# Kernel optimization log

Measured on AMD Instinct MI355X. Metric: run time of the kernel, lower is better.

The kernel has to match this reference:

```python
import jax, jax.numpy as jnp
import numpy as np

B, LQ, LK, H = 8, 2048, 2048, 1024


def setup_inputs() -> dict:
    key = jax.random.key(0)
    kq, kk, kv, km, kw = jax.random.split(key, 5)
    input_Q = jax.random.normal(kq, (B, LQ, H), dtype=jnp.float32)
    input_K = jax.random.normal(kk, (B, LK, H), dtype=jnp.float32)
    input_V = jax.random.normal(kv, (B, LK, H), dtype=jnp.float32)
    mask = jax.random.randint(km, (B, LK), 0, 2, dtype=jnp.int32)
    # learned parameter w_omega [H, H]; scaled init so scores are O(1)-ish
    w_omega = jax.random.normal(kw, (H, H), dtype=jnp.float32) * (H ** -0.5)
    return {"input_Q": input_Q, "input_K": input_K, "input_V": input_V,
            "w_omega": w_omega, "mask": mask}


def reference(input_Q, input_K, input_V, w_omega, mask):
    # att_input = Q @ W : [B, Lq, H]
    att_input = jnp.einsum('bqh,hd->bqd', input_Q, w_omega)
    # scores = att_input @ K^T : [B, Lq, Lk]
    att_scores = jnp.einsum('bqd,bkd->bqk', att_input, input_K)
    # masked fill with -inf where mask == 0 (mask broadcast over query dim)
    neg_inf = jnp.asarray(-jnp.inf, dtype=att_scores.dtype)
    scores = jnp.where(mask[:, None, :] == 0, neg_inf, att_scores)
    probs_softmax = jax.nn.softmax(scores, axis=-1)          # [B, Lq, Lk]
    probs_sigmoid = jax.nn.sigmoid(scores)                   # sigmoid(-inf)=0
    probs_sigmoid_hat = (probs_sigmoid > 0.5).astype(probs_softmax.dtype)
    att_output_softmax = jnp.einsum('bqk,bkh->bqh', probs_softmax, input_V)
    att_output_sigmoid = jnp.einsum('bqk,bkh->bqh', probs_sigmoid_hat, input_V)
    # torch .squeeze(1) is a no-op here since Lq > 1
    return (att_output_softmax, att_output_sigmoid, probs_softmax, probs_sigmoid)
```

## Files before the change

### kernel.cpp

```cpp
#include <hip/hip_runtime.h>
#include <math.h>

#define B_  8
#define LQ_ 2048
#define LK_ 2048
#define H_  1024

#define TAU      4e-3f
#define FIX_CAP  32768
#define FIX_E    8
#define SCL      256.0f
#define SCLQ     16.0f
#define INV_SS   (1.0f / 1048576.0f)

#define KBLK 512

typedef unsigned short ushort_t;
typedef __attribute__((ext_vector_type(8))) _Float16 v8h;
typedef __attribute__((ext_vector_type(8))) short  v8s;
typedef __attribute__((ext_vector_type(4))) float  v4f;
typedef __attribute__((ext_vector_type(4))) float  f4;
typedef __attribute__((ext_vector_type(4))) int    i4;
typedef __attribute__((ext_vector_type(4))) short  s4;

#if defined(__has_builtin)
#if __has_builtin(__builtin_amdgcn_global_load_lds)
#define HAS_GLDS 1
#endif
#endif

__device__ __forceinline__ ushort_t f2bf(float x) {
  unsigned u = __float_as_uint(x);
  u = (u + 0x7FFFu + ((u >> 16) & 1u)) >> 16;
  return (ushort_t)u;
}
__device__ __forceinline__ void split2h(float x, ushort_t& h, ushort_t& l) {
  union { _Float16 f; ushort_t u; } a, b;
  a.f = (_Float16)x;
  b.f = (_Float16)(x - (float)a.f);
  h = a.u; l = b.u;
}

__device__ __forceinline__ void gld_lds16(void* lds_dst, const void* g_src) {
#ifdef HAS_GLDS
  __builtin_amdgcn_global_load_lds((const __attribute__((address_space(1))) void*)g_src,
                                   (__attribute__((address_space(3))) void*)lds_dst,
                                   16, 0, 0);
#else
  *(i4*)lds_dst = *(const i4*)g_src;
#endif
}

__device__ __forceinline__ void xcd_remap(int& bx, int& by, int& bz) {
  const int nx = gridDim.x, ny = gridDim.y;
  const int nwg = nx * ny * gridDim.z;
  const int hwid = bx + nx * (by + ny * bz);
  const int work = (hwid & 7) * (nwg >> 3) + (hwid >> 3);
  bx = work % nx;
  const int t = work / nx;
  by = t % ny;
  bz = t / ny;
}

#define WAIT_VM(n) asm volatile("s_waitcnt vmcnt(" #n ")" ::: "memory")

__global__ __launch_bounds__(256)
void k_prep(const float* __restrict__ Q, const float* __restrict__ K,
            const float* __restrict__ W, const float* __restrict__ V,
            ushort_t* __restrict__ Qhi, ushort_t* __restrict__ Qlo,
            ushort_t* __restrict__ Khi, ushort_t* __restrict__ Klo,
            ushort_t* __restrict__ Wthi, ushort_t* __restrict__ Wtlo,
            ushort_t* __restrict__ Vt, int* __restrict__ cnt) {
  const int blk = blockIdx.x;
  const int tid = threadIdx.x;
  if (blk == 0 && tid == 0) *cnt = 0;

  if (blk < 4096) {
    const int sb = blk & 2047;
    const float* x = (blk < 2048) ? Q : K;
    ushort_t* hi = (blk < 2048) ? Qhi : Khi;
    ushort_t* lo = (blk < 2048) ? Qlo : Klo;
    const float scale = (blk < 2048) ? SCLQ : SCL;
    const int n4 = (int)((size_t)B_ * LQ_ * H_ / 4);
    for (int i = sb * 256 + tid; i < n4; i += 2048 * 256) {
      f4 v = ((const f4*)x)[i];
      s4 h, l;
#pragma unroll
      for (int j = 0; j < 4; j++) {
        ushort_t hb, lb; split2h(v[j] * scale, hb, lb);
        h[j] = (short)hb; l[j] = (short)lb;
      }
      ((s4*)hi)[i] = h;
      ((s4*)lo)[i] = l;
    }
    return;
  }

  __shared__ float t[32][33];
  const int tx = tid & 31, ty = tid >> 5;
  int bx, by, bz, R, C, SPLIT;
  const float* X;
  float scale;
  if (blk < 5120) {
    const int wb = blk - 4096;
    bx = wb & 31; by = wb >> 5; bz = 0; R = H_; C = H_; SPLIT = 1; X = W; scale = SCL;
  } else {
    const int vb = blk - 5120;
    bx = vb & 31; by = (vb >> 5) & 63; bz = vb >> 11; R = LK_; C = H_; SPLIT = 0; X = V; scale = 1.0f;
  }
  const float* Xb = X + (size_t)bz * R * C;
  const int c0 = bx * 32, r0 = by * 32;
#pragma unroll
  for (int i = 0; i < 4; i++)
    t[ty + 8 * i][tx] = Xb[(size_t)(r0 + ty + 8 * i) * C + c0 + tx];
  __syncthreads();
#pragma unroll
  for (int i = 0; i < 4; i++) {
    float v = t[tx][ty + 8 * i] * scale;
    size_t o = (size_t)(c0 + ty + 8 * i) * R + r0 + tx;
    if (SPLIT) {
      ushort_t h, l; split2h(v, h, l);
      Wthi[o] = h; Wtlo[o] = l;
    } else {
      (Vt + (size_t)bz * R * C)[o] = f2bf(v);
    }
  }
}


template <int EPI>
__global__ __launch_bounds__(512, 1)
void gemm_hx2p(const ushort_t* __restrict__ Ahi, const ushort_t* __restrict__ Alo,
               const ushort_t* __restrict__ Bhi, const ushort_t* __restrict__ Blo,
               int KD, long strideAB, long strideBB, int N,
               ushort_t* __restrict__ OutHi, ushort_t* __restrict__ OutLo, long strideOB,
               float* __restrict__ S, float* __restrict__ G, ushort_t* __restrict__ Hatb,
               const int* __restrict__ mask, int* __restrict__ cnt, int* __restrict__ flist) {
  int bx = blockIdx.x, by = blockIdx.y, bz = blockIdx.z;
  xcd_remap(bx, by, bz);
  const int b  = bz;
  const int m0 = by * 256;
  const int n0 = bx * 256;
  const ushort_t* Ah = Ahi + (size_t)b * strideAB + (size_t)m0 * KD;
  const ushort_t* Al = Alo + (size_t)b * strideAB + (size_t)m0 * KD;
  const ushort_t* Bh = Bhi + (size_t)b * strideBB + (size_t)n0 * KD;
  const ushort_t* Bl = Blo + (size_t)b * strideBB + (size_t)n0 * KD;

  __shared__ __attribute__((aligned(16))) char lds[2 * 65536];

  const int tid  = threadIdx.x;
  const int lane = tid & 63;
  const int w    = tid >> 6;
  const int wm   = (w >> 2) * 128;
  const int wn   = (w & 3) * 64;
  const int fr   = lane & 15;
  const int cq   = lane >> 4;

  v4f acc[8][4] = {};

  const int r4 = tid >> 2;
  const int gc = (tid & 3) ^ ((r4 >> 1) & 3);
  const size_t go1 = (size_t)r4 * KD + gc * 8;
  const size_t go2 = (size_t)(r4 + 128) * KD + gc * 8;
  const int lo16 = tid * 16;

#define STG_HX(t_) do {                                                  \
    char* sb_ = lds + ((t_) & 1) * 65536;                                \
    const int kk_ = (t_) * 32;                                           \
    gld_lds16(sb_ + lo16,          Ah + go1 + kk_);                      \
    gld_lds16(sb_ + 8192  + lo16,  Ah + go2 + kk_);                      \
    gld_lds16(sb_ + 16384 + lo16,  Al + go1 + kk_);                      \
    gld_lds16(sb_ + 24576 + lo16,  Al + go2 + kk_);                      \
    gld_lds16(sb_ + 32768 + lo16,  Bh + go1 + kk_);                      \
    gld_lds16(sb_ + 40960 + lo16,  Bh + go2 + kk_);                      \
    gld_lds16(sb_ + 49152 + lo16,  Bl + go1 + kk_);                      \
    gld_lds16(sb_ + 57344 + lo16,  Bl + go2 + kk_);                      \
  } while (0)

  const int nT = KD / 32;
  STG_HX(0);
  for (int t = 0; t < nT; ++t) {
    WAIT_VM(0);
    __builtin_amdgcn_s_barrier();
    if (t + 1 < nT) STG_HX(t + 1);

    const char* sb = lds + (t & 1) * 65536;
    v8h b_h[4], b_l[4];
#pragma unroll
    for (int j = 0; j < 4; j++) {
      const int Rb = wn + j * 16 + fr;
      const int ob = Rb * 64 + ((cq ^ ((Rb >> 1) & 3)) << 4);
      b_h[j] = *(const v8h*)(sb + 32768 + ob);
      b_l[j] = *(const v8h*)(sb + 49152 + ob);
    }
    __builtin_amdgcn_s_setprio(1);
#pragma unroll
    for (int i = 0; i < 8; i++) {
      const int Ra = wm + i * 16 + fr;
      const int oa = Ra * 64 + ((cq ^ ((Ra >> 1) & 3)) << 4);
      v8h a_h = *(const v8h*)(sb + oa);
      v8h a_l = *(const v8h*)(sb + 16384 + oa);
#pragma unroll
      for (int j = 0; j < 4; j++)
        acc[i][j] = __builtin_amdgcn_mfma_f32_16x16x32_f16(a_h, b_h[j], acc[i][j], 0, 0, 0);
#pragma unroll
      for (int j = 0; j < 4; j++)
        acc[i][j] = __builtin_amdgcn_mfma_f32_16x16x32_f16(a_h, b_l[j], acc[i][j], 0, 0, 0);
#pragma unroll
      for (int j = 0; j < 4; j++)
        acc[i][j] = __builtin_amdgcn_mfma_f32_16x16x32_f16(a_l, b_h[j], acc[i][j], 0, 0, 0);
    }
    __builtin_amdgcn_s_setprio(0);
  }
#undef STG_HX

  const int rg = (lane >> 4) * 4;
#pragma unroll
  for (int i = 0; i < 8; i++)
#pragma unroll
    for (int j = 0; j < 4; j++)
#pragma unroll
      for (int r = 0; r < 4; r++) {
        const int grow = m0 + wm + i * 16 + rg + r;
        const int gcol = n0 + wn + j * 16 + fr;
        const float v = acc[i][j][r];
        if (EPI == 0) {
          size_t o = (size_t)b * strideOB + (size_t)grow * N + gcol;
          ushort_t h, l; split2h(v, h, l);
          OutHi[o] = h; OutLo[o] = l;
        } else {
          size_t o = ((size_t)b * LQ_ + grow) * N + gcol;
          const float sv = v * INV_SS;
          S[o] = sv;
          int mk = mask[b * N + gcol];
          const float g = mk ? 1.0f / (1.0f + expf(-sv)) : 0.0f;
          G[o] = g;
          Hatb[o] = (g > 0.5f) ? (ushort_t)0x3F80 : (ushort_t)0;
          if (mk && fabsf(sv) < TAU) {
            int idx = atomicAdd(cnt, 1);
            if (idx < FIX_CAP) flist[idx] = (b << 22) | (grow << 11) | gcol;
          }
        }
      }
}

__global__ __launch_bounds__(256)
void k_fix_blas(const int* __restrict__ cnt, const int* __restrict__ flist,
                const float* __restrict__ Q, const float* __restrict__ Kx,
                const float* __restrict__ W, float* __restrict__ S,
                float* __restrict__ G, ushort_t* __restrict__ Hatb) {
  const int n = min(*cnt, FIX_CAP);
  const int base = blockIdx.x * FIX_E;
  if (base >= n) return;
  const int ne = min(FIX_E, n - base);
  const int tid = threadIdx.x;

  __shared__ float qs[FIX_E][H_];
  __shared__ float aA[FIX_E][H_];
  __shared__ int   ent[FIX_E];

  if (tid < FIX_E) ent[tid] = flist[base + ((tid < ne) ? tid : 0)];
  __syncthreads();

  for (int e = 0; e < FIX_E; e++) {
    const int en = ent[e];
    const int b = en >> 22, q = (en >> 11) & 2047;
    const float* Qr = Q + ((size_t)b * LQ_ + q) * H_;
    for (int i = tid; i < H_; i += 256) qs[e][i] = Qr[i];
  }
  __syncthreads();

  float atot[FIX_E][4];
  float acc[FIX_E][4];
  const float* Wp = W + tid * 4;
#pragma unroll
  for (int blk = 0; blk < 2; blk++) {
    const int h0 = blk * KBLK;
    const int h1 = h0 + KBLK;
#pragma unroll
    for (int e = 0; e < FIX_E; e++)
#pragma unroll
      for (int j = 0; j < 4; j++) acc[e][j] = 0.f;
    for (int h = h0; h < h1; h++) {
      f4 w = *(const f4*)(Wp + (size_t)h * H_);
#pragma unroll
      for (int e = 0; e < FIX_E; e++) {
        const float qv = qs[e][h];
        acc[e][0] = fmaf(qv, w[0], acc[e][0]);
        acc[e][1] = fmaf(qv, w[1], acc[e][1]);
        acc[e][2] = fmaf(qv, w[2], acc[e][2]);
        acc[e][3] = fmaf(qv, w[3], acc[e][3]);
      }
    }
#pragma unroll
    for (int e = 0; e < FIX_E; e++)
#pragma unroll
      for (int j = 0; j < 4; j++)
        atot[e][j] = (blk == 0) ? acc[e][j] : __fadd_rn(atot[e][j], acc[e][j]);
  }
#pragma unroll
  for (int e = 0; e < FIX_E; e++) {
    aA[e][tid * 4 + 0] = atot[e][0];
    aA[e][tid * 4 + 1] = atot[e][1];
    aA[e][tid * 4 + 2] = atot[e][2];
    aA[e][tid * 4 + 3] = atot[e][3];
  }
  __syncthreads();

  if (tid < ne) {
    const int e = tid;
    const int en = ent[e];
    const int b = en >> 22, q = (en >> 11) & 2047, k = en & 2047;
    const float* Kr = Kx + ((size_t)b * LK_ + k) * H_;
    const float* Ar = aA[e];
    float stot = 0.f;
#pragma unroll
    for (int blk = 0; blk < 2; blk++) {
      const int d0 = blk * KBLK;
      const int d1 = d0 + KBLK;
      float a = 0.f;
#pragma unroll 16
      for (int d = d0; d < d1; d++) a = fmaf(Ar[d], Kr[d], a);
      stot = (blk == 0) ? a : __fadd_rn(stot, a);
    }
    size_t o = ((size_t)b * LQ_ + q) * LK_ + k;
    S[o] = stot;
    const float g = 1.0f / (1.0f + expf(-stot));
    G[o] = g;
    Hatb[o] = (g > 0.5f) ? (ushort_t)0x3F80 : (ushort_t)0;
  }
}

__global__ void k_softmax(float* __restrict__ S, const int* __restrict__ mask,
                          ushort_t* __restrict__ Pb) {
  const int row = blockIdx.x;
  const int b   = row >> 11;
  float* Sr = S + (size_t)row * LK_;
  const int* mr = mask + b * LK_;
  const int tid = threadIdx.x;
  const int c0 = tid * 8;

  float v[8]; int mk[8];
  f4 v0 = *(const f4*)&Sr[c0];
  f4 v1 = *(const f4*)&Sr[c0 + 4];
  i4 m0 = *(const i4*)&mr[c0];
  i4 m1 = *(const i4*)&mr[c0 + 4];
#pragma unroll
  for (int j = 0; j < 4; j++) { v[j] = v0[j]; v[4 + j] = v1[j]; mk[j] = m0[j]; mk[4 + j] = m1[j]; }

  float mx = -INFINITY;
#pragma unroll
  for (int j = 0; j < 8; j++) if (mk[j]) mx = fmaxf(mx, v[j]);
#pragma unroll
  for (int off = 32; off; off >>= 1) mx = fmaxf(mx, __shfl_xor(mx, off));
  __shared__ float redm[4], reds[4];
  const int lane = tid & 63, wid = tid >> 6;
  if (lane == 0) redm[wid] = mx;
  __syncthreads();
  mx = fmaxf(fmaxf(redm[0], redm[1]), fmaxf(redm[2], redm[3]));

  float e[8], sum = 0.f;
#pragma unroll
  for (int j = 0; j < 8; j++) { e[j] = mk[j] ? expf(v[j] - mx) : 0.f; sum += e[j]; }
#pragma unroll
  for (int off = 32; off; off >>= 1) sum += __shfl_xor(sum, off);
  if (lane == 0) reds[wid] = sum;
  __syncthreads();
  sum = reds[0] + reds[1] + reds[2] + reds[3];
  const float inv = 1.0f / sum;

  f4 o0, o1;
  v8s pb;
#pragma unroll
  for (int j = 0; j < 4; j++) {
    o0[j] = e[j] * inv; o1[j] = e[4 + j] * inv;
    pb[j] = (short)f2bf(o0[j]); pb[4 + j] = (short)f2bf(o1[j]);
  }
  *(f4*)&Sr[c0] = o0;
  *(f4*)&Sr[c0 + 4] = o1;
  *(v8s*)&Pb[(size_t)row * LK_ + c0] = pb;
}

__global__ __launch_bounds__(512, 1)
void gemm_pv2p(const ushort_t* __restrict__ P, const ushort_t* __restrict__ Hb,
               const ushort_t* __restrict__ Bt,
               float* __restrict__ O0, float* __restrict__ O1) {
  int bx = blockIdx.x, by = blockIdx.y, bz = blockIdx.z;
  xcd_remap(bx, by, bz);
  const int b  = bz;
  const int m0 = by * 128;
  const int n0 = bx * 256;
  const ushort_t* Pa = P  + ((size_t)b * LQ_ + m0) * (size_t)LK_;
  const ushort_t* Ha = Hb + ((size_t)b * LQ_ + m0) * (size_t)LK_;
  const ushort_t* Bb = Bt + ((size_t)b * H_  + n0) * (size_t)LK_;

  __shared__ __attribute__((aligned(16))) char lds[3 * 32768];

  const int tid  = threadIdx.x;
  const int lane = tid & 63;
  const int w    = tid >> 6;
  const int wm   = (w >> 2) * 64;
  const int wn   = (w & 3) * 64;
  const int fr   = lane & 15;
  const int cq   = lane >> 4;

  v4f acc0[4][4] = {}, acc1[4][4] = {};

  const int r4 = tid >> 2;
  const int gc = (tid & 3) ^ ((r4 >> 1) & 3);
  const size_t goA  = (size_t)r4 * LK_ + gc * 8;
  const size_t goB1 = (size_t)(r4 + 128) * LK_ + gc * 8;
  const int lo16 = tid * 16;

#define STG_PV(t_) do {                                                  \
    char* sb = lds + ((t_) % 3) * 32768;                                 \
    const int kk = (t_) * 32;                                            \
    gld_lds16(sb + lo16,          Pa + goA  + kk);                       \
    gld_lds16(sb + 8192 + lo16,   Ha + goA  + kk);                       \
    gld_lds16(sb + 16384 + lo16,  Bb + goA  + kk);                       \
    gld_lds16(sb + 24576 + lo16,  Bb + goB1 + kk);                       \
  } while (0)

  const int nT = LK_ / 32;
  STG_PV(0);
  STG_PV(1);
  for (int t = 0; t < nT; ++t) {
    if (t + 1 < nT) WAIT_VM(4);
    else            WAIT_VM(0);
    __builtin_amdgcn_s_barrier();

    const char* sb = lds + (t % 3) * 32768;
    v8s pf[4], hf[4], bf[4];
#pragma unroll
    for (int i = 0; i < 4; i++) {
      const int Ra = wm + i * 16 + fr;
      const int oa = Ra * 64 + ((cq ^ ((Ra >> 1) & 3)) << 4);
      pf[i] = *(const v8s*)(sb + oa);
      hf[i] = *(const v8s*)(sb + 8192 + oa);
      const int Rb = wn + i * 16 + fr;
      bf[i] = *(const v8s*)(sb + 16384 + Rb * 64 + ((cq ^ ((Rb >> 1) & 3)) << 4));
    }
    if (t + 2 < nT) STG_PV(t + 2);

    __builtin_amdgcn_s_setprio(1);
#pragma unroll
    for (int i = 0; i < 4; i++)
#pragma unroll
      for (int j = 0; j < 4; j++) {
        acc0[i][j] = __builtin_amdgcn_mfma_f32_16x16x32_bf16(pf[i], bf[j], acc0[i][j], 0, 0, 0);
        acc1[i][j] = __builtin_amdgcn_mfma_f32_16x16x32_bf16(hf[i], bf[j], acc1[i][j], 0, 0, 0);
      }
    __builtin_amdgcn_s_setprio(0);
  }
#undef STG_PV

  const int rg = (lane >> 4) * 4;
#pragma unroll
  for (int i = 0; i < 4; i++)
#pragma unroll
    for (int j = 0; j < 4; j++)
#pragma unroll
      for (int r = 0; r < 4; r++) {
        const int grow = m0 + wm + i * 16 + rg + r;
        const int gcol = n0 + wn + j * 16 + fr;
        const size_t o = ((size_t)b * LQ_ + grow) * H_ + gcol;
        O0[o] = acc0[i][j][r];
        O1[o] = acc1[i][j][r];
      }
}

extern "C" void kernel_launch(void* const* d_in, const int* in_sizes, int n_in,
                              void* d_out, int out_size, void* d_ws, size_t ws_size,
                              hipStream_t stream) {
  const float* Q = (const float*)d_in[0];
  const float* K = (const float*)d_in[1];
  const float* V = (const float*)d_in[2];
  const float* W = (const float*)d_in[3];
  const int* mask = (const int*)d_in[4];

  float* out0 = (float*)d_out;
  float* out1 = out0 + (size_t)B_ * LQ_ * H_;
  float* out2 = out1 + (size_t)B_ * LQ_ * H_;
  float* out3 = out2 + (size_t)B_ * LQ_ * LK_;

  const size_t NQ = (size_t)B_ * LQ_ * H_;
  char* ws = (char*)d_ws;
  int* cnt   = (int*)ws;                    ws += 256;
  int* flist = (int*)ws;                    ws += FIX_CAP * 4;
  ushort_t* Qhi = (ushort_t*)ws;            ws += NQ * 2;
  ushort_t* Qlo = (ushort_t*)ws;            ws += NQ * 2;
  ushort_t* Khi = (ushort_t*)ws;            ws += NQ * 2;
  ushort_t* Klo = (ushort_t*)ws;            ws += NQ * 2;
  ushort_t* Ahi = (ushort_t*)ws;            ws += NQ * 2;
  ushort_t* Alo = (ushort_t*)ws;            ws += NQ * 2;
  ushort_t* Vt  = (ushort_t*)ws;            ws += NQ * 2;
  ushort_t* Wthi = (ushort_t*)ws;           ws += (size_t)H_ * H_ * 2;
  ushort_t* Wtlo = (ushort_t*)ws;

  ushort_t* hatb = Qhi;
  ushort_t* Pb   = Ahi;

  k_prep<<<21504, 256, 0, stream>>>(Q, K, W, V, Qhi, Qlo, Khi, Klo,
                                    Wthi, Wtlo, Vt, cnt);

  gemm_hx2p<0><<<dim3(H_ / 256, LQ_ / 256, B_), 512, 0, stream>>>(
      Qhi, Qlo, Wthi, Wtlo, H_, (long)LQ_ * H_, 0L, H_,
      Ahi, Alo, (long)LQ_ * H_, nullptr, nullptr, nullptr, nullptr, nullptr, nullptr);

  gemm_hx2p<1><<<dim3(LK_ / 256, LQ_ / 256, B_), 512, 0, stream>>>(
      Ahi, Alo, Khi, Klo, H_, (long)LQ_ * H_, (long)LK_ * H_, LK_,
      nullptr, nullptr, 0L, out2, out3, hatb, mask, cnt, flist);

  k_fix_blas<<<FIX_CAP / FIX_E, 256, 0, stream>>>(cnt, flist, Q, K, W, out2, out3, hatb);

  k_softmax<<<B_ * LQ_, 256, 0, stream>>>(out2, mask, Pb);

  gemm_pv2p<<<dim3(H_ / 256, LQ_ / 128, B_), 512, 0, stream>>>(Pb, hatb, Vt, out0, out1);
}
```

Measured before the change: 832.3 us.

## Replace double-buffered LDS staging with single buffer in split-fp16 GEMM

```diff
diff --git a/kernel.cpp b/kernel.cpp
--- a/kernel.cpp
+++ b/kernel.cpp
@@ -146,7 +146,7 @@
   const ushort_t* Bh = Bhi + (size_t)b * strideBB + (size_t)n0 * KD;
   const ushort_t* Bl = Blo + (size_t)b * strideBB + (size_t)n0 * KD;
 
-  __shared__ __attribute__((aligned(16))) char lds[2 * 65536];
+  __shared__ __attribute__((aligned(16))) char lds[65536];
 
   const int tid  = threadIdx.x;
   const int lane = tid & 63;
@@ -165,41 +165,38 @@
   const int lo16 = tid * 16;
 
 #define STG_HX(t_) do {                                                  \
-    char* sb_ = lds + ((t_) & 1) * 65536;                                \
     const int kk_ = (t_) * 32;                                           \
-    gld_lds16(sb_ + lo16,          Ah + go1 + kk_);                      \
-    gld_lds16(sb_ + 8192  + lo16,  Ah + go2 + kk_);                      \
-    gld_lds16(sb_ + 16384 + lo16,  Al + go1 + kk_);                      \
-    gld_lds16(sb_ + 24576 + lo16,  Al + go2 + kk_);                      \
-    gld_lds16(sb_ + 32768 + lo16,  Bh + go1 + kk_);                      \
-    gld_lds16(sb_ + 40960 + lo16,  Bh + go2 + kk_);                      \
-    gld_lds16(sb_ + 49152 + lo16,  Bl + go1 + kk_);                      \
-    gld_lds16(sb_ + 57344 + lo16,  Bl + go2 + kk_);                      \
+    gld_lds16(lds + lo16,          Ah + go1 + kk_);                      \
+    gld_lds16(lds + 8192  + lo16,  Ah + go2 + kk_);                      \
+    gld_lds16(lds + 16384 + lo16,  Al + go1 + kk_);                      \
+    gld_lds16(lds + 24576 + lo16,  Al + go2 + kk_);                      \
+    gld_lds16(lds + 32768 + lo16,  Bh + go1 + kk_);                      \
+    gld_lds16(lds + 40960 + lo16,  Bh + go2 + kk_);                      \
+    gld_lds16(lds + 49152 + lo16,  Bl + go1 + kk_);                      \
+    gld_lds16(lds + 57344 + lo16,  Bl + go2 + kk_);                      \
   } while (0)
 
   const int nT = KD / 32;
-  STG_HX(0);
   for (int t = 0; t < nT; ++t) {
+    STG_HX(t);
     WAIT_VM(0);
     __builtin_amdgcn_s_barrier();
-    if (t + 1 < nT) STG_HX(t + 1);
-
-    const char* sb = lds + (t & 1) * 65536;
+
     v8h b_h[4], b_l[4];
 #pragma unroll
     for (int j = 0; j < 4; j++) {
       const int Rb = wn + j * 16 + fr;
       const int ob = Rb * 64 + ((cq ^ ((Rb >> 1) & 3)) << 4);
-      b_h[j] = *(const v8h*)(sb + 32768 + ob);
-      b_l[j] = *(const v8h*)(sb + 49152 + ob);
+      b_h[j] = *(const v8h*)(lds + 32768 + ob);
+      b_l[j] = *(const v8h*)(lds + 49152 + ob);
     }
     __builtin_amdgcn_s_setprio(1);
 #pragma unroll
     for (int i = 0; i < 8; i++) {
       const int Ra = wm + i * 16 + fr;
       const int oa = Ra * 64 + ((cq ^ ((Ra >> 1) & 3)) << 4);
-      v8h a_h = *(const v8h*)(sb + oa);
-      v8h a_l = *(const v8h*)(sb + 16384 + oa);
+      v8h a_h = *(const v8h*)(lds + oa);
+      v8h a_l = *(const v8h*)(lds + 16384 + oa);
 #pragma unroll
       for (int j = 0; j < 4; j++)
         acc[i][j] = __builtin_amdgcn_mfma_f32_16x16x32_f16(a_h, b_h[j], acc[i][j], 0, 0, 0);
@@ -211,6 +208,7 @@
         acc[i][j] = __builtin_amdgcn_mfma_f32_16x16x32_f16(a_l, b_h[j], acc[i][j], 0, 0, 0);
     }
     __builtin_amdgcn_s_setprio(0);
+    __builtin_amdgcn_s_barrier();
   }
 #undef STG_HX
 
```

Result: slower. 893.1 us (+7.3%).
